# Optimization experiments

Hardware: AMD Instinct MI355X
Metric: run time of the kernel (lower is better)

Reference implementation:

```python
import jax, jax.numpy as jnp
import numpy as np

ALPHA = 0.25
GAMMA = 2.0
VAR = jnp.array([0.1, 0.1, 0.2, 0.2, 0.1, 0.1, 0.2, 0.2], dtype=jnp.float32)


def calc_iou(a, b):
    # a: [A,4] anchors, b: [M,4] gt boxes -> IoU [A,M]
    area = (b[:, 2] - b[:, 0]) * (b[:, 3] - b[:, 1])
    iw = jnp.maximum(jnp.minimum(a[:, 2:3], b[:, 2]) - jnp.maximum(a[:, 0:1], b[:, 0]), 0.0)
    ih = jnp.maximum(jnp.minimum(a[:, 3:4], b[:, 3]) - jnp.maximum(a[:, 1:2], b[:, 1]), 0.0)
    ua = jnp.maximum(((a[:, 2] - a[:, 0]) * (a[:, 3] - a[:, 1]))[:, None] + area - iw * ih, 1e-8)
    return iw * ih / ua


def _per_sample(cls_p, reg, anchor, ann1, ann2):
    A = anchor.shape[0]
    M = ann1.shape[0]
    C = cls_p.shape[1]
    clsp = jnp.clip(cls_p, 1e-4, 1.0 - 1e-4)
    iou = calc_iou(anchor, ann1[:, :4])               # [A,M]
    bto = jnp.max(iou, axis=1)                        # best_truth_overlap [A]
    bti = jnp.argmax(iou, axis=1)                     # best_truth_idx [A]
    bpi = jnp.argmax(iou, axis=0)                     # best_prior_idx [M]
    bto = bto.at[bpi].set(2.0)
    owner = jnp.full((A,), -1, jnp.int32).at[bpi].max(jnp.arange(M, dtype=jnp.int32))
    bti = jnp.where(owner >= 0, owner, bti.astype(jnp.int32))
    pos = bto >= 0.5
    neg = bto < 0.4
    assigned = ann1[bti]                              # [A,6]
    labels = assigned[:, 4].astype(jnp.int32)
    onehot = jax.nn.one_hot(labels, C, dtype=clsp.dtype)
    targets = jnp.where(neg[:, None], 0.0, -1.0)
    targets = jnp.where(pos[:, None], onehot, targets)
    af = jnp.where(targets == 1.0, ALPHA, 1.0 - ALPHA)
    fw = af * jnp.where(targets == 1.0, 1.0 - clsp, clsp) ** GAMMA
    bce = -(targets * jnp.log(clsp) + (1.0 - targets) * jnp.log(1.0 - clsp))
    cls_loss = jnp.where(targets != -1.0, fw * bce, 0.0)
    npos = jnp.sum(pos).astype(clsp.dtype)
    cls_out = cls_loss.sum() / jnp.maximum(npos, 1.0)

    aw = anchor[:, 2] - anchor[:, 0]
    ah = anchor[:, 3] - anchor[:, 1]
    acx = anchor[:, 0] + 0.5 * aw
    acy = anchor[:, 1] + 0.5 * ah
    # track-id first-match between frames (replaces nested python loops)
    match = assigned[:, 5][:, None] == ann2[:, 5][None, :]   # [A,M2]
    has = jnp.any(match, axis=1)
    first = jnp.argmax(match, axis=1)
    ann_next = jnp.where(has[:, None], ann2[first], 0.0)     # [A,6]
    gw0 = assigned[:, 2] - assigned[:, 0]
    gh0 = assigned[:, 3] - assigned[:, 1]
    gcx = assigned[:, 0] + 0.5 * gw0
    gcy = assigned[:, 1] + 0.5 * gh0
    gw = jnp.maximum(gw0, 1.0)
    gh = jnp.maximum(gh0, 1.0)
    nw0 = ann_next[:, 2] - ann_next[:, 0]
    nh0 = ann_next[:, 3] - ann_next[:, 1]
    ncx = ann_next[:, 0] + 0.5 * nw0
    ncy = ann_next[:, 1] + 0.5 * nh0
    nw = jnp.maximum(nw0, 1.0)
    nh = jnp.maximum(nh0, 1.0)
    t = jnp.stack([
        (gcx - acx) / aw, (gcy - acy) / ah, jnp.log(gw / aw), jnp.log(gh / ah),
        (ncx - acx) / aw, (ncy - acy) / ah, jnp.log(nw / aw), jnp.log(nh / ah)
    ], axis=1) / VAR                                          # [A,8]
    reg_mask = jnp.concatenate([
        jnp.ones((A, 4), clsp.dtype),
        jnp.broadcast_to(has[:, None], (A, 4)).astype(clsp.dtype)
    ], axis=1)
    diff = jnp.abs(t - reg) * reg_mask
    hub = jnp.where(diff <= 1.0 / 9.0, 0.5 * 9.0 * diff ** 2, diff - 0.5 / 9.0)
    reg_out = jnp.sum(hub * pos[:, None].astype(clsp.dtype)) / jnp.maximum(npos * 8.0, 1.0)
    return cls_out, reg_out


def reference(classifications, regressions, anchors, annotations1, annotations2):
    cl, rl = jax.vmap(_per_sample, in_axes=(0, 0, None, 0, 0))(
        classifications, regressions, anchors[0], annotations1, annotations2)
    return jnp.mean(cl, keepdims=True), jnp.mean(rl, keepdims=True)


def setup_inputs() -> dict:
    key = jax.random.key(0)
    ks = jax.random.split(key, 10)
    B, A, C, M = 8, 100000, 80, 32
    IMG = 512.0

    def rand_boxes(k, prefix):
        k1, k2 = jax.random.split(k)
        ctr = jax.random.uniform(k1, prefix + (2,), jnp.float32, 0.0, IMG)
        wh = jax.random.uniform(k2, prefix + (2,), jnp.float32, 16.0, 128.0)
        return jnp.concatenate([ctr - 0.5 * wh, ctr + 0.5 * wh], axis=-1)

    anchors = rand_boxes(ks[0], (1, A))
    classifications = jax.random.uniform(ks[1], (B, A, C), jnp.float32)
    regressions = jax.random.normal(ks[2], (B, A, 8), jnp.float32) * 0.1

    def make_ann(kb, ki):
        boxes = rand_boxes(kb, (B, M))
        lbl = jax.random.randint(ki, (B, M, 1), 0, C).astype(jnp.float32)
        tid = jax.random.randint(jax.random.fold_in(ki, 1), (B, M, 1), 0, 40).astype(jnp.float32)
        return jnp.concatenate([boxes, lbl, tid], axis=-1)

    annotations1 = make_ann(ks[3], ks[4])
    annotations2 = make_ann(ks[5], ks[6])
    return {"classifications": classifications, "regressions": regressions,
            "anchors": anchors, "annotations1": annotations1, "annotations2": annotations2}
```

## Files before the change

kernel.cpp:

```cpp
#include <hip/hip_runtime.h>

typedef unsigned long long ull;

#define MMAX 64

__global__ void k_iou(const float* __restrict__ anchors, const float* __restrict__ ann1,
                      float* __restrict__ bto, int* __restrict__ bti,
                      ull* __restrict__ part_key, int* __restrict__ part_cnt,
                      int A, int M, int NBLK) {
    __shared__ float s_box[MMAX][4];
    __shared__ float s_area[MMAX];
    __shared__ ull s_part[4][MMAX];
    __shared__ int s_cnt[4];
    const int b = blockIdx.y;
    const int blk = blockIdx.x;
    const int tid = threadIdx.x;
    for (int i = tid; i < M; i += blockDim.x) {
        const float* g = ann1 + ((size_t)b * M + i) * 6;
        float x1 = g[0], y1 = g[1], x2 = g[2], y2 = g[3];
        s_box[i][0] = x1; s_box[i][1] = y1; s_box[i][2] = x2; s_box[i][3] = y2;
        s_area[i] = (x2 - x1) * (y2 - y1);
    }
    __syncthreads();

    const int base = blk * (blockDim.x * 4);
    float ax1[4], ay1[4], ax2[4], ay2[4], aar[4];
    int aidx[4]; bool val[4];
#pragma unroll
    for (int u = 0; u < 4; ++u) {
        int a = base + u * blockDim.x + tid;
        aidx[u] = a; val[u] = (a < A);
        float4 av = make_float4(0.f, 0.f, 0.f, 0.f);
        if (val[u]) av = ((const float4*)anchors)[a];
        ax1[u] = av.x; ay1[u] = av.y; ax2[u] = av.z; ay2[u] = av.w;
        aar[u] = (av.z - av.x) * (av.w - av.y);
    }
    float best[4] = {-1.f, -1.f, -1.f, -1.f};
    int bestj[4] = {0, 0, 0, 0};
    const int lane = tid & 63, wid = tid >> 6;

    for (int j = 0; j < M; ++j) {
        float bx1 = s_box[j][0], by1 = s_box[j][1], bx2 = s_box[j][2], by2 = s_box[j][3];
        float bar = s_area[j];
        ull key = 0ull;
#pragma unroll
        for (int u = 0; u < 4; ++u) {
            float iw = fmaxf(fminf(ax2[u], bx2) - fmaxf(ax1[u], bx1), 0.f);
            float ih = fmaxf(fminf(ay2[u], by2) - fmaxf(ay1[u], by1), 0.f);
            float inter = iw * ih;
            float ua = fmaxf(aar[u] + bar - inter, 1e-8f);
            float iou = inter / ua;
            if (val[u]) {
                if (iou > best[u]) { best[u] = iou; bestj[u] = j; }
                ull k2 = (((ull)__float_as_uint(iou)) << 32) | (ull)(0xFFFFFFFFu - (unsigned)aidx[u]);
                if (k2 > key) key = k2;
            }
        }
#pragma unroll
        for (int off = 32; off > 0; off >>= 1) {
            ull o = __shfl_down(key, off);
            if (o > key) key = o;
        }
        if (lane == 0) s_part[wid][j] = key;
    }
    int cnt = 0;
#pragma unroll
    for (int u = 0; u < 4; ++u) {
        if (val[u]) {
            bto[(size_t)b * A + aidx[u]] = best[u];
            bti[(size_t)b * A + aidx[u]] = bestj[u];
            if (best[u] >= 0.5f) ++cnt;
        }
    }
#pragma unroll
    for (int off = 32; off > 0; off >>= 1) cnt += __shfl_down(cnt, off);
    if (lane == 0) s_cnt[wid] = cnt;
    __syncthreads();
    if (tid < M) {
        ull key = s_part[0][tid];
        if (s_part[1][tid] > key) key = s_part[1][tid];
        if (s_part[2][tid] > key) key = s_part[2][tid];
        if (s_part[3][tid] > key) key = s_part[3][tid];
        part_key[((size_t)b * NBLK + blk) * M + tid] = key;
    }
    if (tid == 0) part_cnt[b * NBLK + blk] = s_cnt[0] + s_cnt[1] + s_cnt[2] + s_cnt[3];
}

__global__ void k_assign(const ull* __restrict__ part_key, const int* __restrict__ part_cnt,
                         float* __restrict__ bto, int* __restrict__ bti,
                         int* __restrict__ npos, float* __restrict__ out,
                         int A, int M, int NBLK) {
    const int b = blockIdx.x;
    const int tid = threadIdx.x;
    __shared__ int s_a[MMAX];
    if (tid < M) {
        ull key = 0ull;
        for (int k = 0; k < NBLK; ++k) {
            ull v = part_key[((size_t)b * NBLK + k) * M + tid];
            if (v > key) key = v;
        }
        s_a[tid] = (int)(0xFFFFFFFFu - (unsigned)(key & 0xFFFFFFFFull));
    }
    __syncthreads();
    int corr = 0;
    if (tid < M) {
        int a = s_a[tid];
        bool owner = true;
        for (int j2 = tid + 1; j2 < M; ++j2)
            if (s_a[j2] == a) owner = false;
        if (owner) {
            float pre = bto[(size_t)b * A + a];
            bto[(size_t)b * A + a] = 2.0f;
            bti[(size_t)b * A + a] = tid;
            if (pre < 0.5f) corr = 1;
        }
    }
    int cnt = corr;
    for (int k = tid; k < NBLK; k += 64) cnt += part_cnt[b * NBLK + k];
#pragma unroll
    for (int off = 32; off > 0; off >>= 1) cnt += __shfl_down(cnt, off);
    if (tid == 0) npos[b] = cnt;
    if (b == 0 && tid == 0) { out[0] = 0.f; out[1] = 0.f; }
}

template <int C4C>
__global__ __launch_bounds__(256, 4)
void k_main(const float* __restrict__ cls, const float* __restrict__ regs,
            const float* __restrict__ anchors,
            const float* __restrict__ ann1, const float* __restrict__ ann2,
            const float* __restrict__ bto, const int* __restrict__ bti,
            const int* __restrict__ npos, float* __restrict__ out,
            int A, int c4_rt, int M, int M2, float invB) {
    const int c4 = (C4C > 0) ? C4C : c4_rt;
    const int b = blockIdx.y;
    const int tid = threadIdx.x;
    __shared__ float s_a1[MMAX * 6];
    __shared__ float s_a2[MMAX * 6];
    for (int i = tid; i < M * 6; i += blockDim.x) s_a1[i] = ann1[(size_t)b * M * 6 + i];
    for (int i = tid; i < M2 * 6; i += blockDim.x) s_a2[i] = ann2[(size_t)b * M2 * 6 + i];
    __syncthreads();

    const int N4 = A * c4;
    const float4* cb = (const float4*)(cls + (size_t)b * A * (c4 * 4));
    const float* btob = bto + (size_t)b * A;
    const int* btib = bti + (size_t)b * A;
    float lsum = 0.f, rsum = 0.f;
    const int stride = gridDim.x * blockDim.x;
    for (int i = blockIdx.x * blockDim.x + tid; i < N4; i += stride) {
        int a = i / c4;
        int c0 = (i - a * c4) * 4;
        float v = btob[a];
        bool pos = (v >= 0.5f), neg = (v < 0.4f);
        if (pos || neg) {
            float4 x = cb[i];
            int label = pos ? (int)s_a1[btib[a] * 6 + 4] : -1;
            float xs[4] = {x.x, x.y, x.z, x.w};
#pragma unroll
            for (int k = 0; k < 4; ++k) {
                float p = fminf(fmaxf(xs[k], 1e-4f), 1.0f - 1e-4f);
                if (pos && (c0 + k) == label) {
                    float q = 1.f - p;
                    lsum += 0.25f * q * q * (-__logf(p));
                } else {
                    lsum += 0.75f * p * p * (-__logf(1.f - p));
                }
            }
        }
        if (pos && c0 == 0) {
            const int ji = btib[a];
            const float* as = &s_a1[ji * 6];
            float4 av = ((const float4*)anchors)[a];
            float aw = av.z - av.x, ah = av.w - av.y;
            float acx = av.x + 0.5f * aw, acy = av.y + 0.5f * ah;
            float gw0 = as[2] - as[0], gh0 = as[3] - as[1];
            float gcx = as[0] + 0.5f * gw0, gcy = as[1] + 0.5f * gh0;
            float gw = fmaxf(gw0, 1.f), gh = fmaxf(gh0, 1.f);
            float t[8];
            t[0] = ((gcx - acx) / aw) / 0.1f;
            t[1] = ((gcy - acy) / ah) / 0.1f;
            t[2] = __logf(gw / aw) / 0.2f;
            t[3] = __logf(gh / ah) / 0.2f;
            int nterm = 4;
            float tid5 = as[5];
            int first = -1;
            for (int j2 = 0; j2 < M2; ++j2) {
                if (s_a2[j2 * 6 + 5] == tid5) { first = j2; break; }
            }
            if (first >= 0) {
                const float* ns = &s_a2[first * 6];
                float nw0 = ns[2] - ns[0], nh0 = ns[3] - ns[1];
                float ncx = ns[0] + 0.5f * nw0, ncy = ns[1] + 0.5f * nh0;
                float nw = fmaxf(nw0, 1.f), nh = fmaxf(nh0, 1.f);
                t[4] = ((ncx - acx) / aw) / 0.1f;
                t[5] = ((ncy - acy) / ah) / 0.1f;
                t[6] = __logf(nw / aw) / 0.2f;
                t[7] = __logf(nh / ah) / 0.2f;
                nterm = 8;
            }
            const float* rg = regs + ((size_t)b * A + a) * 8;
            for (int k = 0; k < nterm; ++k) {
                float d = fabsf(t[k] - rg[k]);
                rsum += (d <= (1.0f / 9.0f)) ? (4.5f * d * d) : (d - (0.5f / 9.0f));
            }
        }
    }
#pragma unroll
    for (int off = 32; off > 0; off >>= 1) {
        lsum += __shfl_down(lsum, off);
        rsum += __shfl_down(rsum, off);
    }
    __shared__ float s_l[4], s_r[4];
    if ((tid & 63) == 0) { s_l[tid >> 6] = lsum; s_r[tid >> 6] = rsum; }
    __syncthreads();
    if (tid == 0) {
        float np_ = (float)npos[b];
        float l = (s_l[0] + s_l[1] + s_l[2] + s_l[3]) / fmaxf(np_, 1.f) * invB;
        float r = (s_r[0] + s_r[1] + s_r[2] + s_r[3]) / fmaxf(np_ * 8.f, 1.f) * invB;
        atomicAdd(&out[0], l);
        atomicAdd(&out[1], r);
    }
}

extern "C" void kernel_launch(void* const* d_in, const int* in_sizes, int n_in,
                              void* d_out, int out_size, void* d_ws, size_t ws_size,
                              hipStream_t stream) {
    const float* cls = (const float*)d_in[0];
    const float* regs = (const float*)d_in[1];
    const float* anchors = (const float*)d_in[2];
    const float* ann1 = (const float*)d_in[3];
    const float* ann2 = (const float*)d_in[4];
    float* out = (float*)d_out;

    const int A = in_sizes[2] / 4;
    const int B = in_sizes[1] / (A * 8);
    const int C = in_sizes[0] / (B * A);
    const int M = in_sizes[3] / (B * 6);
    const int M2 = in_sizes[4] / (B * 6);
    const int NBLK = (A + 1023) / 1024;

    char* ws = (char*)d_ws;
    size_t off = 0;
    float* bto = (float*)(ws + off);     off += (size_t)B * A * sizeof(float);        off = (off + 255) & ~(size_t)255;
    int* bti = (int*)(ws + off);         off += (size_t)B * A * sizeof(int);          off = (off + 255) & ~(size_t)255;
    ull* part_key = (ull*)(ws + off);    off += (size_t)B * NBLK * M * sizeof(ull);   off = (off + 255) & ~(size_t)255;
    int* part_cnt = (int*)(ws + off);    off += (size_t)B * NBLK * sizeof(int);       off = (off + 255) & ~(size_t)255;
    int* npos = (int*)(ws + off);        off += (size_t)B * sizeof(int);

    dim3 g1(NBLK, B);
    k_iou<<<g1, dim3(256), 0, stream>>>(anchors, ann1, bto, bti, part_key, part_cnt, A, M, NBLK);

    k_assign<<<dim3(B), dim3(64), 0, stream>>>(part_key, part_cnt, bto, bti, npos, out, A, M, NBLK);

    dim3 g3(512, B);
    const float invB = 1.0f / (float)B;
    if (C == 80)
        k_main<20><<<g3, dim3(256), 0, stream>>>(cls, regs, anchors, ann1, ann2, bto, bti,
                                                 npos, out, A, C / 4, M, M2, invB);
    else
        k_main<0><<<g3, dim3(256), 0, stream>>>(cls, regs, anchors, ann1, ann2, bto, bti,
                                                npos, out, A, C / 4, M, M2, invB);
}
```

Baseline: 504.9 us.

## Split main loss kernel into branch-free classification and per-anchor regression kernels

The IoU and assignment kernels now precompute a per-anchor code (label for positives, -1 for negatives, -2 for ignored), so the classification kernel reads one int per anchor instead of bto, bti and a shared-memory label lookup. The classification loop becomes branch-free: it always loads the float4, computes background terms masked by a weight, and corrects the single label element. It is also unrolled 4x for memory-level parallelism. Regression moves to its own one-thread-per-anchor kernel, removing the divergent per-float4 regression branch. The cost is an extra workspace array, one more launch, and loading ignored-anchor rows that were previously skipped.

Result: faster. 480.9 us (-4.8%).

```diff
diff --git a/kernel.cpp b/kernel.cpp
--- a/kernel.cpp
+++ b/kernel.cpp
@@ -5,11 +5,12 @@
 #define MMAX 64
 
 __global__ void k_iou(const float* __restrict__ anchors, const float* __restrict__ ann1,
-                      float* __restrict__ bto, int* __restrict__ bti,
+                      float* __restrict__ bto, int* __restrict__ bti, int* __restrict__ acode,
                       ull* __restrict__ part_key, int* __restrict__ part_cnt,
                       int A, int M, int NBLK) {
     __shared__ float s_box[MMAX][4];
     __shared__ float s_area[MMAX];
+    __shared__ float s_lab[MMAX];
     __shared__ ull s_part[4][MMAX];
     __shared__ int s_cnt[4];
     const int b = blockIdx.y;
@@ -20,6 +21,7 @@
         float x1 = g[0], y1 = g[1], x2 = g[2], y2 = g[3];
         s_box[i][0] = x1; s_box[i][1] = y1; s_box[i][2] = x2; s_box[i][3] = y2;
         s_area[i] = (x2 - x1) * (y2 - y1);
+        s_lab[i] = g[4];
     }
     __syncthreads();
 
@@ -67,9 +69,13 @@
 #pragma unroll
     for (int u = 0; u < 4; ++u) {
         if (val[u]) {
-            bto[(size_t)b * A + aidx[u]] = best[u];
+            float bv = best[u];
+            bto[(size_t)b * A + aidx[u]] = bv;
             bti[(size_t)b * A + aidx[u]] = bestj[u];
-            if (best[u] >= 0.5f) ++cnt;
+            int code;
+            if (bv >= 0.5f) { code = (int)s_lab[bestj[u]]; ++cnt; }
+            else code = (bv < 0.4f) ? -1 : -2;
+            acode[(size_t)b * A + aidx[u]] = code;
         }
     }
 #pragma unroll
@@ -87,7 +93,8 @@
 }
 
 __global__ void k_assign(const ull* __restrict__ part_key, const int* __restrict__ part_cnt,
-                         float* __restrict__ bto, int* __restrict__ bti,
+                         const float* __restrict__ ann1,
+                         float* __restrict__ bto, int* __restrict__ bti, int* __restrict__ acode,
                          int* __restrict__ npos, float* __restrict__ out,
                          int A, int M, int NBLK) {
     const int b = blockIdx.x;
@@ -112,6 +119,7 @@
             float pre = bto[(size_t)b * A + a];
             bto[(size_t)b * A + a] = 2.0f;
             bti[(size_t)b * A + a] = tid;
+            acode[(size_t)b * A + a] = (int)ann1[((size_t)b * M + tid) * 6 + 4];
             if (pre < 0.5f) corr = 1;
         }
     }
@@ -123,51 +131,95 @@
     if (b == 0 && tid == 0) { out[0] = 0.f; out[1] = 0.f; }
 }
 
+__device__ __forceinline__ float bg_term(float x) {
+    float p = fminf(fmaxf(x, 1e-4f), 1.0f - 1e-4f);
+    return p * p * (-__logf(1.0f - p));
+}
+
 template <int C4C>
 __global__ __launch_bounds__(256, 4)
-void k_main(const float* __restrict__ cls, const float* __restrict__ regs,
-            const float* __restrict__ anchors,
-            const float* __restrict__ ann1, const float* __restrict__ ann2,
-            const float* __restrict__ bto, const int* __restrict__ bti,
-            const int* __restrict__ npos, float* __restrict__ out,
-            int A, int c4_rt, int M, int M2, float invB) {
+void k_cls(const float* __restrict__ cls, const int* __restrict__ acode,
+           const int* __restrict__ npos, float* __restrict__ out,
+           int A, int c4_rt, float invB) {
     const int c4 = (C4C > 0) ? C4C : c4_rt;
     const int b = blockIdx.y;
     const int tid = threadIdx.x;
+    const int N4 = A * c4;
+    const float4* cb = (const float4*)(cls + (size_t)b * A * (c4 * 4));
+    const int* ac = acode + (size_t)b * A;
+    float lsum = 0.f;
+    const int stride = gridDim.x * blockDim.x;
+    int i = blockIdx.x * blockDim.x + tid;
+
+    for (; i + 3 * stride < N4; i += 4 * stride) {
+        int idx[4], code[4];
+        float4 x[4];
+#pragma unroll
+        for (int u = 0; u < 4; ++u) { idx[u] = i + u * stride; code[u] = ac[idx[u] / c4]; }
+#pragma unroll
+        for (int u = 0; u < 4; ++u) x[u] = cb[idx[u]];
+#pragma unroll
+        for (int u = 0; u < 4; ++u) {
+            float tmp = bg_term(x[u].x) + bg_term(x[u].y) + bg_term(x[u].z) + bg_term(x[u].w);
+            float w = (code[u] == -2) ? 0.f : 0.75f;
+            lsum = fmaf(w, tmp, lsum);
+            int c0 = (idx[u] - (idx[u] / c4) * c4) * 4;
+            int rel = code[u] - c0;
+            if (((unsigned)rel) < 4u) {
+                float xs = (rel == 0) ? x[u].x : (rel == 1) ? x[u].y : (rel == 2) ? x[u].z : x[u].w;
+                float p = fminf(fmaxf(xs, 1e-4f), 1.0f - 1e-4f);
+                float q = 1.f - p;
+                lsum -= 0.75f * p * p * (-__logf(q));
+                lsum += 0.25f * q * q * (-__logf(p));
+            }
+        }
+    }
+    for (; i < N4; i += stride) {
+        int code = ac[i / c4];
+        float4 x = cb[i];
+        float tmp = bg_term(x.x) + bg_term(x.y) + bg_term(x.z) + bg_term(x.w);
+        float w = (code == -2) ? 0.f : 0.75f;
+        lsum = fmaf(w, tmp, lsum);
+        int c0 = (i - (i / c4) * c4) * 4;
+        int rel = code - c0;
+        if (((unsigned)rel) < 4u) {
+            float xs = (rel == 0) ? x.x : (rel == 1) ? x.y : (rel == 2) ? x.z : x.w;
+            float p = fminf(fmaxf(xs, 1e-4f), 1.0f - 1e-4f);
+            float q = 1.f - p;
+            lsum -= 0.75f * p * p * (-__logf(q));
+            lsum += 0.25f * q * q * (-__logf(p));
+        }
+    }
+#pragma unroll
+    for (int off = 32; off > 0; off >>= 1) lsum += __shfl_down(lsum, off);
+    __shared__ float s_l[4];
+    if ((tid & 63) == 0) s_l[tid >> 6] = lsum;
+    __syncthreads();
+    if (tid == 0) {
+        float np_ = (float)npos[b];
+        atomicAdd(&out[0], (s_l[0] + s_l[1] + s_l[2] + s_l[3]) / fmaxf(np_, 1.f) * invB);
+    }
+}
+
+__global__ void k_reg(const float* __restrict__ anchors, const float* __restrict__ ann1,
+                      const float* __restrict__ ann2, const float* __restrict__ regs,
+                      const float* __restrict__ bto, const int* __restrict__ bti,
+                      const int* __restrict__ npos, float* __restrict__ out,
+                      int A, int M, int M2, float invB) {
     __shared__ float s_a1[MMAX * 6];
     __shared__ float s_a2[MMAX * 6];
+    const int b = blockIdx.y;
+    const int tid = threadIdx.x;
     for (int i = tid; i < M * 6; i += blockDim.x) s_a1[i] = ann1[(size_t)b * M * 6 + i];
     for (int i = tid; i < M2 * 6; i += blockDim.x) s_a2[i] = ann2[(size_t)b * M2 * 6 + i];
     __syncthreads();
 
-    const int N4 = A * c4;
-    const float4* cb = (const float4*)(cls + (size_t)b * A * (c4 * 4));
-    const float* btob = bto + (size_t)b * A;
-    const int* btib = bti + (size_t)b * A;
-    float lsum = 0.f, rsum = 0.f;
-    const int stride = gridDim.x * blockDim.x;
-    for (int i = blockIdx.x * blockDim.x + tid; i < N4; i += stride) {
-        int a = i / c4;
-        int c0 = (i - a * c4) * 4;
-        float v = btob[a];
-        bool pos = (v >= 0.5f), neg = (v < 0.4f);
-        if (pos || neg) {
-            float4 x = cb[i];
-            int label = pos ? (int)s_a1[btib[a] * 6 + 4] : -1;
-            float xs[4] = {x.x, x.y, x.z, x.w};
-#pragma unroll
-            for (int k = 0; k < 4; ++k) {
-                float p = fminf(fmaxf(xs[k], 1e-4f), 1.0f - 1e-4f);
-                if (pos && (c0 + k) == label) {
-                    float q = 1.f - p;
-                    lsum += 0.25f * q * q * (-__logf(p));
-                } else {
-                    lsum += 0.75f * p * p * (-__logf(1.f - p));
-                }
-            }
-        }
-        if (pos && c0 == 0) {
-            const int ji = btib[a];
+    const int a = blockIdx.x * blockDim.x + tid;
+    float sum = 0.f;
+    if (a < A) {
+        float v = bto[(size_t)b * A + a];
+        if (v >= 0.5f) {
+            const int ji = bti[(size_t)b * A + a];
             const float* as = &s_a1[ji * 6];
             float4 av = ((const float4*)anchors)[a];
             float aw = av.z - av.x, ah = av.w - av.y;
@@ -200,24 +252,21 @@
             const float* rg = regs + ((size_t)b * A + a) * 8;
             for (int k = 0; k < nterm; ++k) {
                 float d = fabsf(t[k] - rg[k]);
-                rsum += (d <= (1.0f / 9.0f)) ? (4.5f * d * d) : (d - (0.5f / 9.0f));
-            }
-        }
-    }
-#pragma unroll
-    for (int off = 32; off > 0; off >>= 1) {
-        lsum += __shfl_down(lsum, off);
-        rsum += __shfl_down(rsum, off);
-    }
-    __shared__ float s_l[4], s_r[4];
-    if ((tid & 63) == 0) { s_l[tid >> 6] = lsum; s_r[tid >> 6] = rsum; }
+                sum += (d <= (1.0f / 9.0f)) ? (4.5f * d * d) : (d - (0.5f / 9.0f));
+            }
+        }
+    }
+#pragma unroll
+    for (int off = 32; off > 0; off >>= 1) sum += __shfl_down(sum, off);
+    __shared__ float s_rs[4];
+    if ((tid & 63) == 0) s_rs[tid >> 6] = sum;
     __syncthreads();
     if (tid == 0) {
-        float np_ = (float)npos[b];
-        float l = (s_l[0] + s_l[1] + s_l[2] + s_l[3]) / fmaxf(np_, 1.f) * invB;
-        float r = (s_r[0] + s_r[1] + s_r[2] + s_r[3]) / fmaxf(np_ * 8.f, 1.f) * invB;
-        atomicAdd(&out[0], l);
-        atomicAdd(&out[1], r);
+        float s = s_rs[0] + s_rs[1] + s_rs[2] + s_rs[3];
+        if (s != 0.f) {
+            float np_ = (float)npos[b];
+            atomicAdd(&out[1], s / fmaxf(np_ * 8.f, 1.f) * invB);
+        }
     }
 }
 
@@ -242,21 +291,23 @@
     size_t off = 0;
     float* bto = (float*)(ws + off);     off += (size_t)B * A * sizeof(float);        off = (off + 255) & ~(size_t)255;
     int* bti = (int*)(ws + off);         off += (size_t)B * A * sizeof(int);          off = (off + 255) & ~(size_t)255;
+    int* acode = (int*)(ws + off);       off += (size_t)B * A * sizeof(int);          off = (off + 255) & ~(size_t)255;
     ull* part_key = (ull*)(ws + off);    off += (size_t)B * NBLK * M * sizeof(ull);   off = (off + 255) & ~(size_t)255;
     int* part_cnt = (int*)(ws + off);    off += (size_t)B * NBLK * sizeof(int);       off = (off + 255) & ~(size_t)255;
     int* npos = (int*)(ws + off);        off += (size_t)B * sizeof(int);
 
     dim3 g1(NBLK, B);
-    k_iou<<<g1, dim3(256), 0, stream>>>(anchors, ann1, bto, bti, part_key, part_cnt, A, M, NBLK);
-
-    k_assign<<<dim3(B), dim3(64), 0, stream>>>(part_key, part_cnt, bto, bti, npos, out, A, M, NBLK);
+    k_iou<<<g1, dim3(256), 0, stream>>>(anchors, ann1, bto, bti, acode, part_key, part_cnt, A, M, NBLK);
+
+    k_assign<<<dim3(B), dim3(64), 0, stream>>>(part_key, part_cnt, ann1, bto, bti, acode, npos, out, A, M, NBLK);
 
     dim3 g3(512, B);
     const float invB = 1.0f / (float)B;
     if (C == 80)
-        k_main<20><<<g3, dim3(256), 0, stream>>>(cls, regs, anchors, ann1, ann2, bto, bti,
-                                                 npos, out, A, C / 4, M, M2, invB);
+        k_cls<20><<<g3, dim3(256), 0, stream>>>(cls, acode, npos, out, A, C / 4, invB);
     else
-        k_main<0><<<g3, dim3(256), 0, stream>>>(cls, regs, anchors, ann1, ann2, bto, bti,
-                                                npos, out, A, C / 4, M, M2, invB);
-}
+        k_cls<0><<<g3, dim3(256), 0, stream>>>(cls, acode, npos, out, A, C / 4, invB);
+
+    dim3 g4((A + 255) / 256, B);
+    k_reg<<<g4, dim3(256), 0, stream>>>(anchors, ann1, ann2, regs, bto, bti, npos, out, A, M, M2, invB);
+}
```
